# Performance work log

Measured on AMD Instinct MI355X. Metric: run time of the kernel, lower is better.

Reference implementation:

```python
import jax, jax.numpy as jnp
import numpy as np

N = 100000        # num nodes
F_IN = 256        # params['topo_feature']
C = 128           # params['num_edge'] (hidden & GCN channels)
E = 1_600_000     # num edges (avg degree 16)


def setup_inputs() -> dict:
    key = jax.random.key(0)
    k = jax.random.split(key, 6)
    x = jax.random.normal(k[0], (N, F_IN), dtype=jnp.float32)
    edge_index = jax.random.randint(k[1], (2, E), 0, N, dtype=jnp.int32)
    # fc1: Linear(F_IN, C)
    W1 = jax.random.normal(k[2], (C, F_IN), dtype=jnp.float32) * (1.0 / np.sqrt(F_IN))
    b1 = jnp.zeros((C,), dtype=jnp.float32)
    # GCNConv linear: Linear(C, C, bias=False) weight + separate bias added post-aggregation
    W2 = jax.random.normal(k[3], (C, C), dtype=jnp.float32) * (1.0 / np.sqrt(C))
    b2 = jnp.zeros((C,), dtype=jnp.float32)
    return {"x": x, "edge_index": edge_index, "W1": W1, "b1": b1, "W2": W2, "b2": b2}


def reference(x, edge_index, W1, b1, W2, b2):
    # fc1 + relu
    h = jax.nn.relu(x @ W1.T + b1)                       # [N, C]
    # GCNConv: transform, add self-loops, sym-normalize, scatter-add
    z = h @ W2.T                                         # [N, C]
    loop = jnp.arange(N, dtype=edge_index.dtype)
    src = jnp.concatenate([edge_index[0], loop])         # [E+N]
    dst = jnp.concatenate([edge_index[1], loop])         # [E+N]
    deg = jax.ops.segment_sum(jnp.ones_like(dst, jnp.float32), dst, num_segments=N)
    dinv = jnp.where(deg > 0, jax.lax.rsqrt(jnp.maximum(deg, 1.0)), 0.0)
    norm = (dinv[src] * dinv[dst])[:, None]              # [E+N, 1]
    out = jax.ops.segment_sum(z[src] * norm, dst, num_segments=N) + b2
    return out
```

## Files before the change

kernel.cpp:

```cpp
#include <hip/hip_runtime.h>

typedef unsigned short ushort;
typedef __bf16 bf16x8 __attribute__((ext_vector_type(8)));
typedef float f32x4 __attribute__((ext_vector_type(4)));

#define F_IN 256
#define CCH  128
#define BSH  7
#define BNODES 128
#define NBUCK 1024
#define CHUNK 2048

__device__ __forceinline__ ushort f2bf(float f) {
    union { float f; unsigned i; } u; u.f = f;
    unsigned r = u.i + 0x7fffu + ((u.i >> 16) & 1u);
    return (ushort)(r >> 16);
}
__device__ __forceinline__ float2 bf2f2(unsigned u) {
    union { unsigned i; float f; } lo, hi;
    lo.i = u << 16;
    hi.i = u & 0xffff0000u;
    return make_float2(lo.f, hi.f);
}
__device__ __forceinline__ void gload_lds16(const void* g, void* l) {
    __builtin_amdgcn_global_load_lds((const __attribute__((address_space(1))) unsigned*)g,
                                     (__attribute__((address_space(3))) unsigned*)l, 16, 0, 0);
}

__global__ __launch_bounds__(256)
void hist_cvt(const int* __restrict__ dst, int* __restrict__ histC, int* __restrict__ histT,
              int E, int nchunks, int ncp,
              const float* __restrict__ W1, const float* __restrict__ W2,
              ushort* __restrict__ w1b, ushort* __restrict__ w2b)
{
    const int blk = blockIdx.x, t = threadIdx.x;
    if (blk >= nchunks) {
        int i = (blk - nchunks) * 256 + t;
        if (i < CCH * F_IN) {
            int c  = i & 31;
            int cs = c ^ (((i >> 9) & 3) << 3);
            w1b[(i & ~31) | cs] = f2bf(W1[i]);
        } else {
            int j = i - CCH * F_IN;
            if (j < CCH * CCH) w2b[j] = f2bf(W2[j]);
        }
        return;
    }
    __shared__ int h[NBUCK];
    for (int i = t; i < NBUCK; i += 256) h[i] = 0;
    __syncthreads();
    int cb = blk * CHUNK, ce = min(cb + CHUNK, E);
    for (int e = cb + t; e < ce; e += 256)
        atomicAdd(&h[dst[e] >> BSH], 1);
    __syncthreads();
    const int ncp16 = ncp * 16;
    for (int i = t; i < NBUCK; i += 256) {
        int v = h[i];
        histC[blk * NBUCK + i] = v;
        histT[(i >> 4) * ncp16 + blk * 16 + (i & 15)] = v;
    }
}

__global__ __launch_bounds__(1024)
void scan_buckets(int* __restrict__ histT, int* __restrict__ btot, int nchunks, int ncp)
{
    const int w = threadIdx.x >> 6;
    const int b = blockIdx.x * 16 + w;
    const int lane = threadIdx.x & 63;
    const int tb = blockIdx.x * (ncp * 16) + w;
    int carry = 0;
    for (int c = 0; c < nchunks; c += 64) {
        int idx = c + lane;
        int v = (idx < nchunks) ? histT[tb + idx * 16] : 0;
        int inc = v;
#pragma unroll
        for (int off = 1; off < 64; off <<= 1) {
            int x = __shfl_up(inc, off, 64);
            if (lane >= off) inc += x;
        }
        if (idx < nchunks) histT[tb + idx * 16] = carry + inc - v;
        carry += __shfl(inc, 63, 64);
    }
    if (lane == 0) btot[b] = carry;
}

__device__ __forceinline__ void partition_body(unsigned* smem4,
    const int* __restrict__ src, const int* __restrict__ dst,
    const int* __restrict__ histC, const int* __restrict__ histPre,
    const int* __restrict__ btot, int* __restrict__ gbase,
    unsigned* __restrict__ pairs, int E, int ncp, int blk)
{
    int* lcur = (int*)smem4;
    int* off  = lcur + NBUCK;
    int* wsum = off + NBUCK;
    const int t = threadIdx.x;
    const int wv = t >> 6, lane = t & 63;

    int4 cv = *(const int4*)&histC[blk * NBUCK + 4 * t];
    int tsum = cv.x + cv.y + cv.z + cv.w;
    int inc = tsum;
#pragma unroll
    for (int o = 1; o < 64; o <<= 1) {
        int x = __shfl_up(inc, o, 64);
        if (lane >= o) inc += x;
    }
    if (lane == 63) wsum[wv] = inc;
    __syncthreads();
    int woff = 0;
    if (wv > 0) woff += wsum[0];
    if (wv > 1) woff += wsum[1];
    if (wv > 2) woff += wsum[2];
    int l0 = woff + inc - tsum, l1 = l0 + cv.x, l2 = l1 + cv.y, l3 = l2 + cv.z;
    lcur[4 * t] = l0; lcur[4 * t + 1] = l1; lcur[4 * t + 2] = l2; lcur[4 * t + 3] = l3;

    int4 bt = *(const int4*)&btot[4 * t];
    int bsum = bt.x + bt.y + bt.z + bt.w;
    int binc = bsum;
#pragma unroll
    for (int o = 1; o < 64; o <<= 1) {
        int x = __shfl_up(binc, o, 64);
        if (lane >= o) binc += x;
    }
    __syncthreads();
    if (lane == 63) wsum[wv] = binc;
    __syncthreads();
    int bwoff = 0;
    if (wv > 0) bwoff += wsum[0];
    if (wv > 1) bwoff += wsum[1];
    if (wv > 2) bwoff += wsum[2];
    int b0 = bwoff + binc - bsum, b1 = b0 + bt.x, b2 = b1 + bt.y, b3 = b2 + bt.z;
    if (blk == 0) {
        *(int4*)&gbase[4 * t] = make_int4(b0, b1, b2, b3);
        if (t == 255) gbase[NBUCK] = b3 + bt.w;
    }
    int4 pf = *(const int4*)&histPre[(t >> 2) * (ncp * 16) + blk * 16 + (t & 3) * 4];
    off[4 * t]     = b0 + pf.x - l0;
    off[4 * t + 1] = b1 + pf.y - l1;
    off[4 * t + 2] = b2 + pf.z - l2;
    off[4 * t + 3] = b3 + pf.w - l3;
    __syncthreads();

    const int cb = blk * CHUNK, ce = min(cb + CHUNK, E);
    for (int e = cb + t; e < ce; e += 256) {
        int d = dst[e];
        int b = d >> BSH;
        unsigned packed = ((unsigned)src[e] << BSH) | (unsigned)(d & (BNODES - 1));
        int p = atomicAdd(&lcur[b], 1);
        pairs[off[b] + p] = packed;
    }
}

__device__ __forceinline__ void csr_body(unsigned* smem4,
    const unsigned* __restrict__ pairs, const int* __restrict__ base,
    int* __restrict__ row_start, float* __restrict__ dinv,
    unsigned* __restrict__ csr, int N, int E, int b, int lastb)
{
    int* deg  = (int*)smem4;
    int* cur  = deg + BNODES;
    int* wsum = cur + BNODES;
    const int t = threadIdx.x;
    if (t < BNODES) deg[t] = 0;
    __syncthreads();
    const int rb = base[b], re = base[b + 1];
    for (int e = rb + t; e < re; e += 256)
        atomicAdd(&deg[pairs[e] & (BNODES - 1)], 1);
    __syncthreads();
    int v = (t < BNODES) ? deg[t] : 0;
    int inc = v;
#pragma unroll
    for (int o = 1; o < 64; o <<= 1) {
        int x = __shfl_up(inc, o, 64);
        if ((t & 63) >= o) inc += x;
    }
    if (t < BNODES && (t & 63) == 63) wsum[t >> 6] = inc;
    __syncthreads();
    const int n0 = b << BSH;
    if (t < BNODES) {
        int excl = inc - v + ((t >= 64) ? wsum[0] : 0);
        cur[t] = rb + excl;
        if (n0 + t < N) {
            row_start[n0 + t] = rb + excl;
            dinv[n0 + t] = rsqrtf((float)v + 1.0f);
        }
    }
    if (b == lastb && t == 0) row_start[N] = E;
    __syncthreads();
    for (int e = rb + t; e < re; e += 256) {
        unsigned p = pairs[e];
        int slot = atomicAdd(&cur[p & (BNODES - 1)], 1);
        csr[slot] = p >> BSH;
    }
}

__device__ __forceinline__ void gemm_body(unsigned* smem4,
    const float* __restrict__ X, const ushort* __restrict__ W1b,
    const ushort* __restrict__ W2b, const float* __restrict__ b1,
    ushort* __restrict__ Zq, int M, int m0)
{
    ushort* smem = (ushort*)smem4;
    ushort* Ht = smem;
    const int tid  = threadIdx.x;
    const int wave = tid >> 6, lane = tid & 63;
    const int wm = (wave & 1) * 64, wn = (wave >> 1) * 64;
    const int lr = lane & 15, lq = lane >> 4;

    const int arow = tid >> 2;
    const int aq   = tid & 3;

    float4 ar[2][2];
    auto loadX = [&](int k0) {
#pragma unroll
        for (int it = 0; it < 2; it++) {
            int grow = min(m0 + arow + it * 64, M - 1);
            const float* p = &X[(long)grow * F_IN + k0 + aq * 8];
            ar[it][0] = *(const float4*)p;
            ar[it][1] = *(const float4*)(p + 4);
        }
    };
    auto writeA = [&](ushort* As) {
#pragma unroll
        for (int it = 0; it < 2; it++) {
            int row = arow + it * 64;
            ushort u[8] = { f2bf(ar[it][0].x), f2bf(ar[it][0].y), f2bf(ar[it][0].z), f2bf(ar[it][0].w),
                            f2bf(ar[it][1].x), f2bf(ar[it][1].y), f2bf(ar[it][1].z), f2bf(ar[it][1].w) };
            *(uint4*)&As[row * 32 + ((aq ^ ((row >> 1) & 3)) << 3)] = *(uint4*)u;
        }
    };
    auto stageB = [&](int k0, ushort* Bs) {
#pragma unroll
        for (int it = 0; it < 2; it++) {
            int r0 = wave * 32 + it * 16;
            const ushort* g = &W1b[(long)(r0 + (lane >> 2)) * F_IN + k0 + (lane & 3) * 8];
            gload_lds16(g, &Bs[r0 * 32]);
        }
    };

    f32x4 acc[4][4] = {};
    loadX(0);
    stageB(0, smem + 4096);
    writeA(smem);
    __syncthreads();
    for (int k0 = 0; k0 < F_IN; k0 += 32) {
        const int cur = (k0 >> 5) & 1;
        ushort* As = smem + cur * 8192;
        ushort* Bs = As + 4096;
        const bool more = (k0 + 32 < F_IN);
        if (more) {
            stageB(k0 + 32, smem + (cur ^ 1) * 8192 + 4096);
            loadX(k0 + 32);
        }
        bf16x8 af[4], bfr[4];
#pragma unroll
        for (int t4 = 0; t4 < 4; t4++) {
            int ra = wm + t4 * 16 + lr;
            int rb = wn + t4 * 16 + lr;
            af[t4]  = *(bf16x8*)&As[ra * 32 + ((lq ^ ((ra >> 1) & 3)) << 3)];
            bfr[t4] = *(bf16x8*)&Bs[rb * 32 + ((lq ^ ((rb >> 1) & 3)) << 3)];
        }
#pragma unroll
        for (int i = 0; i < 4; i++)
#pragma unroll
            for (int j = 0; j < 4; j++)
                acc[i][j] = __builtin_amdgcn_mfma_f32_16x16x32_bf16(af[i], bfr[j], acc[i][j], 0, 0, 0);
        if (more) writeA(smem + (cur ^ 1) * 8192);
        __syncthreads();
    }

    uint4 wb[2][4];
#pragma unroll
    for (int t4 = 0; t4 < 4; t4++)
        wb[0][t4] = *(const uint4*)&W2b[(long)(wn + t4 * 16 + lr) * CCH + lq * 8];

    {
        float bv[4];
#pragma unroll
        for (int j = 0; j < 4; j++) bv[j] = b1[wn + j * 16 + lr];
#pragma unroll
        for (int i = 0; i < 4; i++)
#pragma unroll
            for (int r = 0; r < 4; r++) {
                int row = wm + i * 16 + lq * 4 + r;
                int rx  = (row & 7) << 3;
#pragma unroll
                for (int j = 0; j < 4; j++)
                    Ht[row * 128 + ((wn + j * 16 + lr) ^ rx)] = f2bf(fmaxf(acc[i][j][r] + bv[j], 0.f));
            }
    }
    __syncthreads();

    f32x4 acc2[4][4] = {};
#pragma unroll
    for (int kk = 0; kk < 4; kk++) {
        const int k0 = kk * 32;
        if (kk < 3) {
#pragma unroll
            for (int t4 = 0; t4 < 4; t4++)
                wb[(kk + 1) & 1][t4] =
                    *(const uint4*)&W2b[(long)(wn + t4 * 16 + lr) * CCH + k0 + 32 + lq * 8];
        }
        bf16x8 af[4];
#pragma unroll
        for (int t4 = 0; t4 < 4; t4++) {
            int ra = wm + t4 * 16 + lr;
            af[t4] = *(bf16x8*)&Ht[ra * 128 + ((k0 + lq * 8) ^ ((ra & 7) << 3))];
        }
#pragma unroll
        for (int i = 0; i < 4; i++)
#pragma unroll
            for (int j = 0; j < 4; j++)
                acc2[i][j] = __builtin_amdgcn_mfma_f32_16x16x32_bf16(af[i], *(bf16x8*)&wb[kk & 1][j],
                                                                     acc2[i][j], 0, 0, 0);
    }
    __syncthreads();

#pragma unroll
    for (int i = 0; i < 4; i++)
#pragma unroll
        for (int r = 0; r < 4; r++) {
            int row = wm + i * 16 + lq * 4 + r;
            int rx  = (row & 7) << 3;
#pragma unroll
            for (int j = 0; j < 4; j++)
                Ht[row * 128 + ((wn + j * 16 + lr) ^ rx)] = f2bf(acc2[i][j][r]);
        }
    __syncthreads();
    {
        int colq = tid & 15, row0 = tid >> 4;
#pragma unroll
        for (int i = 0; i < 8; i++) {
            int row = row0 + i * 16;
            if (m0 + row < M)
                *(uint4*)&Zq[(long)(m0 + row) * CCH + colq * 8] =
                    *(uint4*)&Ht[row * 128 + ((colq * 8) ^ ((row & 7) << 3))];
        }
    }
}

__global__ __launch_bounds__(256)
void u_part_gemm(const int* __restrict__ src, const int* __restrict__ dst,
                 const int* __restrict__ histC, const int* __restrict__ histPre,
                 const int* __restrict__ btot, int* __restrict__ gbase,
                 unsigned* __restrict__ pairs, int E, int ncp, int nchunks,
                 const float* __restrict__ X, const ushort* __restrict__ W1b,
                 const ushort* __restrict__ W2b, const float* __restrict__ b1,
                 ushort* __restrict__ Zq, int M)
{
    __shared__ unsigned smem4[8192];
    const int bid = blockIdx.x;
    if (bid < nchunks) {
        const int x = bid & 7, i = bid >> 3;
        const int q = nchunks >> 3, r = nchunks & 7;
        const int chunk = (x < r) ? x * (q + 1) + i : r * (q + 1) + (x - r) * q + i;
        partition_body(smem4, src, dst, histC, histPre, btot, gbase, pairs, E, ncp, chunk);
    } else {
        gemm_body(smem4, X, W1b, W2b, b1, Zq, M, (bid - nchunks) * 128);
    }
}

__global__ __launch_bounds__(256)
void u_csr_gemm(const unsigned* __restrict__ pairs, const int* __restrict__ base,
                int* __restrict__ row_start, float* __restrict__ dinv,
                unsigned* __restrict__ csr, int N, int E, int nbuck, int ngA,
                const float* __restrict__ X, const ushort* __restrict__ W1b,
                const ushort* __restrict__ W2b, const float* __restrict__ b1,
                ushort* __restrict__ Zq, int M)
{
    __shared__ unsigned smem4[8192];
    const int bid = blockIdx.x;
    if (bid < nbuck)
        csr_body(smem4, pairs, base, row_start, dinv, csr, N, E, bid, nbuck - 1);
    else
        gemm_body(smem4, X, W1b, W2b, b1, Zq, M, (ngA + bid - nbuck) * 128);
}

__global__ __launch_bounds__(256)
void gather_nodes(const unsigned* __restrict__ zq, const unsigned* __restrict__ csr,
                  const int* __restrict__ row_start, const float* __restrict__ dinv,
                  const float* __restrict__ b2, float* __restrict__ out, int N)
{
    const int node = blockIdx.x * 4 + (threadIdx.x >> 6);
    const int lane = threadIdx.x & 63;
    if (node >= N) return;

    const float di = dinv[node];
    float2 zs = bf2f2(zq[(long)node * 64 + lane]);
    float acc0 = di * zs.x, acc1 = di * zs.y;

    const int rs = row_start[node];
    const int re = row_start[node + 1];
    int j = rs;
    for (; j + 16 <= re; j += 16) {
        unsigned sI[16], zv[16];
        float dv[16];
#pragma unroll
        for (int q = 0; q < 16; q++) sI[q] = csr[j + q];
#pragma unroll
        for (int q = 0; q < 16; q++) zv[q] = zq[(long)sI[q] * 64 + lane];
#pragma unroll
        for (int q = 0; q < 16; q++) dv[q] = dinv[sI[q]];
#pragma unroll
        for (int q = 0; q < 16; q++) { float2 f = bf2f2(zv[q]); acc0 += dv[q] * f.x; acc1 += dv[q] * f.y; }
    }
    for (; j + 4 <= re; j += 4) {
        unsigned sI[4], zv[4];
        float dv[4];
#pragma unroll
        for (int q = 0; q < 4; q++) sI[q] = csr[j + q];
#pragma unroll
        for (int q = 0; q < 4; q++) zv[q] = zq[(long)sI[q] * 64 + lane];
#pragma unroll
        for (int q = 0; q < 4; q++) dv[q] = dinv[sI[q]];
#pragma unroll
        for (int q = 0; q < 4; q++) { float2 f = bf2f2(zv[q]); acc0 += dv[q] * f.x; acc1 += dv[q] * f.y; }
    }
    for (; j < re; j++) {
        unsigned s = csr[j];
        float ds = dinv[s];
        float2 f = bf2f2(zq[(long)s * 64 + lane]);
        acc0 += ds * f.x; acc1 += ds * f.y;
    }

    float2 o;
    o.x = b2[lane * 2 + 0] + di * acc0;
    o.y = b2[lane * 2 + 1] + di * acc1;
    *(float2*)&out[(long)node * CCH + lane * 2] = o;
}

extern "C" void kernel_launch(void* const* d_in, const int* in_sizes, int n_in,
                              void* d_out, int out_size, void* d_ws, size_t ws_size,
                              hipStream_t stream)
{
    const float* x  = (const float*)d_in[0];
    const int*   ei = (const int*)d_in[1];
    const float* W1 = (const float*)d_in[2];
    const float* b1 = (const float*)d_in[3];
    const float* W2 = (const float*)d_in[4];
    const float* b2 = (const float*)d_in[5];
    float* out = (float*)d_out;

    const int N = in_sizes[0] / F_IN;
    const int E = in_sizes[1] / 2;
    const int* src = ei;
    const int* dst = ei + E;

    const int nchunks = (E + CHUNK - 1) / CHUNK;
    const int ncp     = (nchunks + 63) & ~63;
    const int nbuck   = (N + BNODES - 1) / BNODES;
    const int ngrid   = (N + 127) / 128;
    const int ngA     = (ngrid + 1) / 2;
    const int ngB     = ngrid - ngA;
    const int ncvt    = (CCH * F_IN + CCH * CCH + 255) / 256;

    char* ws = (char*)d_ws;
    ushort* zq    = (ushort*)ws;   ws += (size_t)N * CCH * 2;
    ushort* w1b   = (ushort*)ws;   ws += (size_t)CCH * F_IN * 2;
    ushort* w2b   = (ushort*)ws;   ws += (size_t)CCH * CCH * 2;
    unsigned* prs = (unsigned*)ws; ws += (size_t)E * 4;
    unsigned* csr = (unsigned*)ws; ws += (size_t)E * 4;
    int* rstart   = (int*)ws;      ws += ((size_t)N + 1) * 4;
    float* dinv   = (float*)ws;    ws += (size_t)N * 4;
    int* histC    = (int*)ws;      ws += (size_t)nchunks * NBUCK * 4;
    int* histT    = (int*)ws;      ws += (size_t)NBUCK * ncp * 4;
    int* btot     = (int*)ws;      ws += NBUCK * 4;
    int* gbase    = (int*)ws;      ws += (NBUCK + 1) * 4;

    hist_cvt<<<nchunks + ncvt, 256, 0, stream>>>(dst, histC, histT, E, nchunks, ncp, W1, W2, w1b, w2b);
    scan_buckets<<<NBUCK / 16, 1024, 0, stream>>>(histT, btot, nchunks, ncp);
    u_part_gemm<<<nchunks + ngA, 256, 0, stream>>>(src, dst, histC, histT, btot, gbase, prs,
                                                   E, ncp, nchunks, x, w1b, w2b, b1, zq, N);
    u_csr_gemm<<<nbuck + ngB, 256, 0, stream>>>(prs, gbase, rstart, dinv, csr, N, E,
                                                nbuck, ngA, x, w1b, w2b, b1, zq, N);
    gather_nodes<<<(N + 3) / 4, 256, 0, stream>>>((const unsigned*)zq, csr, rstart, dinv, b2, out, N);
}
```

Baseline: 344.7 us.

## Spread GEMM tiles across histogram, partition and CSR stages; trim gather unroll

```diff
diff --git a/kernel.cpp b/kernel.cpp
--- a/kernel.cpp
+++ b/kernel.cpp
@@ -28,25 +28,26 @@
 }
 
 __global__ __launch_bounds__(256)
-void hist_cvt(const int* __restrict__ dst, int* __restrict__ histC, int* __restrict__ histT,
-              int E, int nchunks, int ncp,
-              const float* __restrict__ W1, const float* __restrict__ W2,
-              ushort* __restrict__ w1b, ushort* __restrict__ w2b)
-{
-    const int blk = blockIdx.x, t = threadIdx.x;
-    if (blk >= nchunks) {
-        int i = (blk - nchunks) * 256 + t;
-        if (i < CCH * F_IN) {
-            int c  = i & 31;
-            int cs = c ^ (((i >> 9) & 3) << 3);
-            w1b[(i & ~31) | cs] = f2bf(W1[i]);
-        } else {
-            int j = i - CCH * F_IN;
-            if (j < CCH * CCH) w2b[j] = f2bf(W2[j]);
-        }
-        return;
-    }
-    __shared__ int h[NBUCK];
+void cvt_w(const float* __restrict__ W1, const float* __restrict__ W2,
+           ushort* __restrict__ w1b, ushort* __restrict__ w2b)
+{
+    int i = blockIdx.x * 256 + threadIdx.x;
+    if (i < CCH * F_IN) {
+        int c  = i & 31;
+        int cs = c ^ (((i >> 9) & 3) << 3);
+        w1b[(i & ~31) | cs] = f2bf(W1[i]);
+    } else {
+        int j = i - CCH * F_IN;
+        if (j < CCH * CCH) w2b[j] = f2bf(W2[j]);
+    }
+}
+
+__device__ __forceinline__ void hist_body(unsigned* smem4,
+    const int* __restrict__ dst, int* __restrict__ histC, int* __restrict__ histT,
+    int E, int ncp, int blk)
+{
+    int* h = (int*)smem4;
+    const int t = threadIdx.x;
     for (int i = t; i < NBUCK; i += 256) h[i] = 0;
     __syncthreads();
     int cb = blk * CHUNK, ce = min(cb + CHUNK, E);
@@ -337,10 +338,25 @@
 }
 
 __global__ __launch_bounds__(256)
+void u_hist_gemm(const int* __restrict__ dst, int* __restrict__ histC, int* __restrict__ histT,
+                 int E, int ncp, int nchunks,
+                 const float* __restrict__ X, const ushort* __restrict__ W1b,
+                 const ushort* __restrict__ W2b, const float* __restrict__ b1,
+                 ushort* __restrict__ Zq, int M)
+{
+    __shared__ unsigned smem4[8192];
+    const int bid = blockIdx.x;
+    if (bid < nchunks)
+        hist_body(smem4, dst, histC, histT, E, ncp, bid);
+    else
+        gemm_body(smem4, X, W1b, W2b, b1, Zq, M, (bid - nchunks) * 128);
+}
+
+__global__ __launch_bounds__(256)
 void u_part_gemm(const int* __restrict__ src, const int* __restrict__ dst,
                  const int* __restrict__ histC, const int* __restrict__ histPre,
                  const int* __restrict__ btot, int* __restrict__ gbase,
-                 unsigned* __restrict__ pairs, int E, int ncp, int nchunks,
+                 unsigned* __restrict__ pairs, int E, int ncp, int nchunks, int ngA,
                  const float* __restrict__ X, const ushort* __restrict__ W1b,
                  const ushort* __restrict__ W2b, const float* __restrict__ b1,
                  ushort* __restrict__ Zq, int M)
@@ -353,14 +369,14 @@
         const int chunk = (x < r) ? x * (q + 1) + i : r * (q + 1) + (x - r) * q + i;
         partition_body(smem4, src, dst, histC, histPre, btot, gbase, pairs, E, ncp, chunk);
     } else {
-        gemm_body(smem4, X, W1b, W2b, b1, Zq, M, (bid - nchunks) * 128);
+        gemm_body(smem4, X, W1b, W2b, b1, Zq, M, (ngA + bid - nchunks) * 128);
     }
 }
 
 __global__ __launch_bounds__(256)
 void u_csr_gemm(const unsigned* __restrict__ pairs, const int* __restrict__ base,
                 int* __restrict__ row_start, float* __restrict__ dinv,
-                unsigned* __restrict__ csr, int N, int E, int nbuck, int ngA,
+                unsigned* __restrict__ csr, int N, int E, int nbuck, int ngAB,
                 const float* __restrict__ X, const ushort* __restrict__ W1b,
                 const ushort* __restrict__ W2b, const float* __restrict__ b1,
                 ushort* __restrict__ Zq, int M)
@@ -370,7 +386,7 @@
     if (bid < nbuck)
         csr_body(smem4, pairs, base, row_start, dinv, csr, N, E, bid, nbuck - 1);
     else
-        gemm_body(smem4, X, W1b, W2b, b1, Zq, M, (ngA + bid - nbuck) * 128);
+        gemm_body(smem4, X, W1b, W2b, b1, Zq, M, (ngAB + bid - nbuck) * 128);
 }
 
 __global__ __launch_bounds__(256)
@@ -389,29 +405,17 @@
     const int rs = row_start[node];
     const int re = row_start[node + 1];
     int j = rs;
-    for (; j + 16 <= re; j += 16) {
-        unsigned sI[16], zv[16];
-        float dv[16];
-#pragma unroll
-        for (int q = 0; q < 16; q++) sI[q] = csr[j + q];
-#pragma unroll
-        for (int q = 0; q < 16; q++) zv[q] = zq[(long)sI[q] * 64 + lane];
-#pragma unroll
-        for (int q = 0; q < 16; q++) dv[q] = dinv[sI[q]];
-#pragma unroll
-        for (int q = 0; q < 16; q++) { float2 f = bf2f2(zv[q]); acc0 += dv[q] * f.x; acc1 += dv[q] * f.y; }
-    }
-    for (; j + 4 <= re; j += 4) {
-        unsigned sI[4], zv[4];
-        float dv[4];
-#pragma unroll
-        for (int q = 0; q < 4; q++) sI[q] = csr[j + q];
-#pragma unroll
-        for (int q = 0; q < 4; q++) zv[q] = zq[(long)sI[q] * 64 + lane];
-#pragma unroll
-        for (int q = 0; q < 4; q++) dv[q] = dinv[sI[q]];
-#pragma unroll
-        for (int q = 0; q < 4; q++) { float2 f = bf2f2(zv[q]); acc0 += dv[q] * f.x; acc1 += dv[q] * f.y; }
+    for (; j + 8 <= re; j += 8) {
+        unsigned sI[8], zv[8];
+        float dv[8];
+#pragma unroll
+        for (int q = 0; q < 8; q++) sI[q] = csr[j + q];
+#pragma unroll
+        for (int q = 0; q < 8; q++) dv[q] = dinv[sI[q]];
+#pragma unroll
+        for (int q = 0; q < 8; q++) zv[q] = zq[(long)sI[q] * 64 + lane];
+#pragma unroll
+        for (int q = 0; q < 8; q++) { float2 f = bf2f2(zv[q]); acc0 += dv[q] * f.x; acc1 += dv[q] * f.y; }
     }
     for (; j < re; j++) {
         unsigned s = csr[j];
@@ -447,8 +451,9 @@
     const int ncp     = (nchunks + 63) & ~63;
     const int nbuck   = (N + BNODES - 1) / BNODES;
     const int ngrid   = (N + 127) / 128;
-    const int ngA     = (ngrid + 1) / 2;
-    const int ngB     = ngrid - ngA;
+    const int ngA     = ngrid / 4;
+    const int ngB     = (ngrid * 9) / 20;
+    const int ngC     = ngrid - ngA - ngB;
     const int ncvt    = (CCH * F_IN + CCH * CCH + 255) / 256;
 
     char* ws = (char*)d_ws;
@@ -464,11 +469,13 @@
     int* btot     = (int*)ws;      ws += NBUCK * 4;
     int* gbase    = (int*)ws;      ws += (NBUCK + 1) * 4;
 
-    hist_cvt<<<nchunks + ncvt, 256, 0, stream>>>(dst, histC, histT, E, nchunks, ncp, W1, W2, w1b, w2b);
+    cvt_w<<<ncvt, 256, 0, stream>>>(W1, W2, w1b, w2b);
+    u_hist_gemm<<<nchunks + ngA, 256, 0, stream>>>(dst, histC, histT, E, ncp, nchunks,
+                                                   x, w1b, w2b, b1, zq, N);
     scan_buckets<<<NBUCK / 16, 1024, 0, stream>>>(histT, btot, nchunks, ncp);
-    u_part_gemm<<<nchunks + ngA, 256, 0, stream>>>(src, dst, histC, histT, btot, gbase, prs,
-                                                   E, ncp, nchunks, x, w1b, w2b, b1, zq, N);
-    u_csr_gemm<<<nbuck + ngB, 256, 0, stream>>>(prs, gbase, rstart, dinv, csr, N, E,
-                                                nbuck, ngA, x, w1b, w2b, b1, zq, N);
+    u_part_gemm<<<nchunks + ngB, 256, 0, stream>>>(src, dst, histC, histT, btot, gbase, prs,
+                                                   E, ncp, nchunks, ngA, x, w1b, w2b, b1, zq, N);
+    u_csr_gemm<<<nbuck + ngC, 256, 0, stream>>>(prs, gbase, rstart, dinv, csr, N, E,
+                                                nbuck, ngA + ngB, x, w1b, w2b, b1, zq, N);
     gather_nodes<<<(N + 3) / 4, 256, 0, stream>>>((const unsigned*)zq, csr, rstart, dinv, b2, out, N);
 }
```

Measured after the change: 332.5 us. 1.04x faster.
